# Optimization experiments

Measured on AMD Instinct MI355X. Metric: run time of the kernel, lower is better.

Reference implementation:

```python
import jax, jax.numpy as jnp
import numpy as np

B, T, F, H = 64, 2048, 128, 32  # batch, seq_len, input_features, lstm hidden


def setup_inputs() -> dict:
    key = jax.random.key(0)
    ks = jax.random.split(key, 4)
    X = jax.random.normal(ks[0], (B, T, F), dtype=jnp.float32)
    # combined gate weights, order (i, f, g, o) as in flax.linen.LSTMCell
    Wx = jax.random.normal(ks[1], (F, 4 * H), dtype=jnp.float32) / np.float32(np.sqrt(F))
    Wh = jax.random.normal(ks[2], (H, 4 * H), dtype=jnp.float32) / np.float32(np.sqrt(H))
    b = jnp.zeros((4 * H,), dtype=jnp.float32)
    Wd = jax.random.normal(ks[3], (H, 1), dtype=jnp.float32) / np.float32(np.sqrt(H))
    bd = jnp.zeros((1,), dtype=jnp.float32)
    return {"X": X, "Wx": Wx, "Wh": Wh, "b": b, "Wd": Wd, "bd": bd}


def reference(X, Wx, Wh, b, Wd, bd):
    # Precompute input->gate projections for all timesteps in one GEMM.
    xg = jnp.einsum('btf,fg->btg', X, Wx) + b  # [B, T, 4H]

    def step(carry, xg_t):
        c, h = carry
        g = xg_t + h @ Wh  # [B, 4H]
        i, f, gc, o = jnp.split(g, 4, axis=-1)
        c = jax.nn.sigmoid(f) * c + jax.nn.sigmoid(i) * jnp.tanh(gc)
        h = jax.nn.sigmoid(o) * jnp.tanh(c)
        return (c, h), None

    zeros = jnp.zeros((X.shape[0], H), X.dtype)
    (c_T, h_T), _ = jax.lax.scan(step, (zeros, zeros), jnp.swapaxes(xg, 0, 1))
    # Dense(1) applied to outputs, then last timestep selected == Dense on h_T
    return h_T @ Wd + bd  # [B, 1]
```

## Files before the change

### kernel.cpp

```cpp
#include <hip/hip_runtime.h>
#include <math.h>

#define BB 64
#define TT 2048
#define FF 128
#define HH 32
#define GG 128

#define S1f (-1.4426950408889634f)
#define S2f (-2.8853900817779268f)

__global__ __launch_bounds__(256) void xg_gemm(const float* __restrict__ X,
                                               const float* __restrict__ Wx,
                                               const float* __restrict__ bias,
                                               float* __restrict__ xgT) {
    __shared__ float XL[64 * 32];
    __shared__ float WL[32 * 128];
    const int tid = threadIdx.x;
    const int row0 = blockIdx.x * 64;
    const int j0 = (tid & 15) * 8;
    const int r0 = (tid >> 4) * 4;

    float acc[4][8];
#pragma unroll
    for (int r = 0; r < 4; ++r)
#pragma unroll
        for (int jj = 0; jj < 8; ++jj) acc[r][jj] = 0.f;

    for (int f0 = 0; f0 < FF; f0 += 32) {
        __syncthreads();
        {
            const float4* src = (const float4*)(Wx + f0 * GG);
            float4* dst = (float4*)WL;
            dst[tid]       = src[tid];
            dst[tid + 256] = src[tid + 256];
            dst[tid + 512] = src[tid + 512];
            dst[tid + 768] = src[tid + 768];
        }
        {
            int lin = tid * 4;
            int row = lin >> 5;
            int fi  = lin & 31;
            ((float4*)XL)[tid] =
                *(const float4*)(X + (size_t)(row0 + row) * FF + f0 + fi);
            lin = (tid + 256) * 4;
            row = lin >> 5;
            fi  = lin & 31;
            ((float4*)XL)[tid + 256] =
                *(const float4*)(X + (size_t)(row0 + row) * FF + f0 + fi);
        }
        __syncthreads();
#pragma unroll 4
        for (int fi = 0; fi < 32; ++fi) {
            float xv[4];
#pragma unroll
            for (int r = 0; r < 4; ++r) xv[r] = XL[(r0 + r) * 32 + fi];
            float4 w0 = *(float4*)&WL[fi * GG + j0];
            float4 w1 = *(float4*)&WL[fi * GG + j0 + 4];
            float w[8] = {w0.x, w0.y, w0.z, w0.w, w1.x, w1.y, w1.z, w1.w};
#pragma unroll
            for (int r = 0; r < 4; ++r)
#pragma unroll
                for (int jj = 0; jj < 8; ++jj)
                    acc[r][jj] = fmaf(xv[r], w[jj], acc[r][jj]);
        }
    }
    const int b  = row0 >> 11;
    const int t0 = (row0 & 2047) + r0;
    float bl[8];
#pragma unroll
    for (int jj = 0; jj < 8; ++jj) bl[jj] = bias[j0 + jj];
#pragma unroll
    for (int jj = 0; jj < 8; ++jj) {
        const int j = j0 + jj;
        const float sc = (j >= 64 && j < 96) ? S2f : S1f;
        float4 o;
        o.x = (acc[0][jj] + bl[jj]) * sc;
        o.y = (acc[1][jj] + bl[jj]) * sc;
        o.z = (acc[2][jj] + bl[jj]) * sc;
        o.w = (acc[3][jj] + bl[jj]) * sc;
        *(float4*)(xgT + ((size_t)b * GG + j) * TT + t0) = o;
    }
}

__device__ __forceinline__ float rcp_(float x) { return __builtin_amdgcn_rcpf(x); }
__device__ __forceinline__ float exp2_(float x) { return __builtin_amdgcn_exp2f(x); }

__global__ __launch_bounds__(64) void lstm_rec(const float* __restrict__ xgT,
                                               const float* __restrict__ Wh,
                                               const float* __restrict__ Wd,
                                               const float* __restrict__ bd,
                                               float* __restrict__ out) {
    const int b = blockIdx.x;
    const int l = threadIdx.x;
    const bool lo = (l < HH);

    const float scx = S1f;
    const float scy = lo ? S2f : S1f;
    float2 wh[HH];
#pragma unroll
    for (int k = 0; k < HH; ++k)
        wh[k] = make_float2(Wh[k * GG + l] * scx, Wh[k * GG + l + 64] * scy);

    const float A1 = lo ? 2.f : 1.f;
    const float B1 = lo ? -1.f : 0.f;

    float h = 0.f;
    float c = 0.f;

    const float* pX = xgT + ((size_t)b * GG + l) * TT;
    const float* pY = xgT + ((size_t)b * GG + l + 64) * TT;

    float4 curX = *(const float4*)(pX);
    float4 curY = *(const float4*)(pY);
    float4 nxtX = *(const float4*)(pX + 4);
    float4 nxtY = *(const float4*)(pY + 4);

    auto step = [&](float xi, float xy) __attribute__((always_inline)) {
        float ax[4] = {xi, 0.f, 0.f, 0.f};
        float ay[4] = {xy, 0.f, 0.f, 0.f};
#pragma unroll
        for (int kc = 0; kc < 4; ++kc) {
#pragma unroll
            for (int k = 0; k < 8; ++k) {
                const int kk = kc * 8 + k;
                float hk = __uint_as_float(
                    __builtin_amdgcn_readlane(__float_as_uint(h), kk));
                ax[kc] = fmaf(hk, wh[kk].x, ax[kc]);
                ay[kc] = fmaf(hk, wh[kk].y, ay[kc]);
            }
        }
        float a0 = (ax[0] + ax[1]) + (ax[2] + ax[3]);
        float a1 = (ay[0] + ay[1]) + (ay[2] + ay[3]);

        float act0 = rcp_(1.f + exp2_(a0));
        float act1 = fmaf(A1, rcp_(1.f + exp2_(a1)), B1);

        auto pq = __builtin_amdgcn_permlane32_swap(__float_as_uint(act0),
                                                   __float_as_uint(act1), false, false);
        auto uv = __builtin_amdgcn_permlane32_swap(__float_as_uint(act1),
                                                   __float_as_uint(act0), false, false);
        float p = __uint_as_float(pq[0]);
        float q = __uint_as_float(pq[1]);
        float u = __uint_as_float(uv[0]);
        float v = __uint_as_float(uv[1]);

        float f_all = lo ? q : act0;
        float o_all = lo ? v : act1;
        c = fmaf(f_all, c, u * p);
        float tc = fmaf(2.f, rcp_(1.f + exp2_(c * S2f)), -1.f);
        h = o_all * tc;
    };

#pragma unroll 1
    for (int t4 = 0; t4 < TT; t4 += 4) {
        float4 uX = curX, uY = curY;
        curX = nxtX; curY = nxtY;
        if (t4 + 8 < TT) {
            nxtX = *(const float4*)(pX + t4 + 8);
            nxtY = *(const float4*)(pY + t4 + 8);
        }
        step(uX.x, uY.x);
        step(uX.y, uY.y);
        step(uX.z, uY.z);
        step(uX.w, uY.w);
    }

    float contrib = h * Wd[l & (HH - 1)];
#pragma unroll
    for (int off = 32; off >= 1; off >>= 1)
        contrib += __shfl_xor(contrib, off, 64);
    if (l == 0) out[b] = fmaf(0.5f, contrib, bd[0]);
}

extern "C" void kernel_launch(void* const* d_in, const int* in_sizes, int n_in,
                              void* d_out, int out_size, void* d_ws, size_t ws_size,
                              hipStream_t stream) {
    const float* X    = (const float*)d_in[0];
    const float* Wx   = (const float*)d_in[1];
    const float* Wh   = (const float*)d_in[2];
    const float* bias = (const float*)d_in[3];
    const float* Wd   = (const float*)d_in[4];
    const float* bd   = (const float*)d_in[5];
    float* out = (float*)d_out;
    float* xgT = (float*)d_ws;

    hipLaunchKernelGGL(xg_gemm, dim3((BB * TT) / 64), dim3(256), 0, stream,
                       X, Wx, bias, xgT);
    hipLaunchKernelGGL(lstm_rec, dim3(BB), dim3(64), 0, stream,
                       xgT, Wh, Wd, bd, out);
}
```

Measured before the change: 523.1 us.

## Use packed fp16 dot2 for recurrent matvec and interleave two batches per wave

Recurrent weights are packed into fp16 pairs, and h is paired with its neighbouring lane via DPP, so the 32-term matvec becomes 16 fdot2 ops with half the readlanes. Each wave now runs two independent batch sequences whose steps are interleaved to hide dependency latency, and the launch uses half as many blocks. This lowers per-step instruction count and latency on the serial critical path. The cost is fp16 rounding of weights and hidden state, which lowers accuracy.

```diff
diff --git a/kernel.cpp b/kernel.cpp
--- a/kernel.cpp
+++ b/kernel.cpp
@@ -9,6 +9,21 @@
 
 #define S1f (-1.4426950408889634f)
 #define S2f (-2.8853900817779268f)
+
+typedef _Float16 half2_t __attribute__((ext_vector_type(2)));
+
+__device__ __forceinline__ unsigned h2u(half2_t v) {
+    unsigned u; __builtin_memcpy(&u, &v, 4); return u;
+}
+__device__ __forceinline__ half2_t u2h(unsigned u) {
+    half2_t v; __builtin_memcpy(&v, &u, 4); return v;
+}
+__device__ __forceinline__ half2_t pkrtz(float a, float b) {
+    auto r = __builtin_amdgcn_cvt_pkrtz(a, b);
+    half2_t v; __builtin_memcpy(&v, &r, 4); return v;
+}
+__device__ __forceinline__ float rcp_(float x) { return __builtin_amdgcn_rcpf(x); }
+__device__ __forceinline__ float exp2_(float x) { return __builtin_amdgcn_exp2f(x); }
 
 __global__ __launch_bounds__(256) void xg_gemm(const float* __restrict__ X,
                                                const float* __restrict__ Wx,
@@ -83,52 +98,64 @@
     }
 }
 
-__device__ __forceinline__ float rcp_(float x) { return __builtin_amdgcn_rcpf(x); }
-__device__ __forceinline__ float exp2_(float x) { return __builtin_amdgcn_exp2f(x); }
-
 __global__ __launch_bounds__(64) void lstm_rec(const float* __restrict__ xgT,
                                                const float* __restrict__ Wh,
                                                const float* __restrict__ Wd,
                                                const float* __restrict__ bd,
                                                float* __restrict__ out) {
-    const int b = blockIdx.x;
     const int l = threadIdx.x;
     const bool lo = (l < HH);
+    const int b0 = blockIdx.x * 2;
+    const int b1 = b0 + 1;
 
     const float scx = S1f;
     const float scy = lo ? S2f : S1f;
-    float2 wh[HH];
-#pragma unroll
-    for (int k = 0; k < HH; ++k)
-        wh[k] = make_float2(Wh[k * GG + l] * scx, Wh[k * GG + l + 64] * scy);
+    half2_t whx[16], why[16];
+#pragma unroll
+    for (int k = 0; k < 16; ++k) {
+        float w0 = Wh[(2 * k) * GG + l] * scx;
+        float w1 = Wh[(2 * k + 1) * GG + l] * scx;
+        whx[k] = pkrtz(w0, w1);
+        float v0 = Wh[(2 * k) * GG + l + 64] * scy;
+        float v1 = Wh[(2 * k + 1) * GG + l + 64] * scy;
+        why[k] = pkrtz(v0, v1);
+    }
 
     const float A1 = lo ? 2.f : 1.f;
     const float B1 = lo ? -1.f : 0.f;
 
-    float h = 0.f;
-    float c = 0.f;
-
-    const float* pX = xgT + ((size_t)b * GG + l) * TT;
-    const float* pY = xgT + ((size_t)b * GG + l + 64) * TT;
-
-    float4 curX = *(const float4*)(pX);
-    float4 curY = *(const float4*)(pY);
-    float4 nxtX = *(const float4*)(pX + 4);
-    float4 nxtY = *(const float4*)(pY + 4);
-
-    auto step = [&](float xi, float xy) __attribute__((always_inline)) {
+    float hA = 0.f, cA = 0.f;
+    float hB = 0.f, cB = 0.f;
+
+    const float* pXA = xgT + ((size_t)b0 * GG + l) * TT;
+    const float* pYA = xgT + ((size_t)b0 * GG + l + 64) * TT;
+    const float* pXB = xgT + ((size_t)b1 * GG + l) * TT;
+    const float* pYB = xgT + ((size_t)b1 * GG + l + 64) * TT;
+
+    float4 curXA = *(const float4*)(pXA);
+    float4 curYA = *(const float4*)(pYA);
+    float4 curXB = *(const float4*)(pXB);
+    float4 curYB = *(const float4*)(pYB);
+    float4 nxtXA = *(const float4*)(pXA + 4);
+    float4 nxtYA = *(const float4*)(pYA + 4);
+    float4 nxtXB = *(const float4*)(pXB + 4);
+    float4 nxtYB = *(const float4*)(pYB + 4);
+
+    auto step = [&](float& h, float& c, float xi, float xy)
+        __attribute__((always_inline)) {
+        unsigned hu = __float_as_uint(h);
+        unsigned hxu = (unsigned)__builtin_amdgcn_mov_dpp(
+            (int)hu, 0xB1 , 0xF, 0xF, true);
+        half2_t hp = pkrtz(h, __uint_as_float(hxu));
+        unsigned hpu = h2u(hp);
+
         float ax[4] = {xi, 0.f, 0.f, 0.f};
         float ay[4] = {xy, 0.f, 0.f, 0.f};
 #pragma unroll
-        for (int kc = 0; kc < 4; ++kc) {
-#pragma unroll
-            for (int k = 0; k < 8; ++k) {
-                const int kk = kc * 8 + k;
-                float hk = __uint_as_float(
-                    __builtin_amdgcn_readlane(__float_as_uint(h), kk));
-                ax[kc] = fmaf(hk, wh[kk].x, ax[kc]);
-                ay[kc] = fmaf(hk, wh[kk].y, ay[kc]);
-            }
+        for (int k = 0; k < 16; ++k) {
+            half2_t s = u2h(__builtin_amdgcn_readlane(hpu, 2 * k));
+            ax[k & 3] = __builtin_amdgcn_fdot2(s, whx[k], ax[k & 3], false);
+            ay[k & 3] = __builtin_amdgcn_fdot2(s, why[k], ay[k & 3], false);
         }
         float a0 = (ax[0] + ax[1]) + (ax[2] + ax[3]);
         float a1 = (ay[0] + ay[1]) + (ay[2] + ay[3]);
@@ -154,23 +181,32 @@
 
 #pragma unroll 1
     for (int t4 = 0; t4 < TT; t4 += 4) {
-        float4 uX = curX, uY = curY;
-        curX = nxtX; curY = nxtY;
+        float4 uXA = curXA, uYA = curYA, uXB = curXB, uYB = curYB;
+        curXA = nxtXA; curYA = nxtYA; curXB = nxtXB; curYB = nxtYB;
         if (t4 + 8 < TT) {
-            nxtX = *(const float4*)(pX + t4 + 8);
-            nxtY = *(const float4*)(pY + t4 + 8);
-        }
-        step(uX.x, uY.x);
-        step(uX.y, uY.y);
-        step(uX.z, uY.z);
-        step(uX.w, uY.w);
-    }
-
-    float contrib = h * Wd[l & (HH - 1)];
-#pragma unroll
-    for (int off = 32; off >= 1; off >>= 1)
-        contrib += __shfl_xor(contrib, off, 64);
-    if (l == 0) out[b] = fmaf(0.5f, contrib, bd[0]);
+            nxtXA = *(const float4*)(pXA + t4 + 8);
+            nxtYA = *(const float4*)(pYA + t4 + 8);
+            nxtXB = *(const float4*)(pXB + t4 + 8);
+            nxtYB = *(const float4*)(pYB + t4 + 8);
+        }
+        step(hA, cA, uXA.x, uYA.x);  step(hB, cB, uXB.x, uYB.x);
+        step(hA, cA, uXA.y, uYA.y);  step(hB, cB, uXB.y, uYB.y);
+        step(hA, cA, uXA.z, uYA.z);  step(hB, cB, uXB.z, uYB.z);
+        step(hA, cA, uXA.w, uYA.w);  step(hB, cB, uXB.w, uYB.w);
+    }
+
+    const float wd = Wd[l & (HH - 1)];
+    float ca = hA * wd;
+    float cb = hB * wd;
+#pragma unroll
+    for (int off = 32; off >= 1; off >>= 1) {
+        ca += __shfl_xor(ca, off, 64);
+        cb += __shfl_xor(cb, off, 64);
+    }
+    if (l == 0) {
+        out[b0] = fmaf(0.5f, ca, bd[0]);
+        out[b1] = fmaf(0.5f, cb, bd[0]);
+    }
 }
 
 extern "C" void kernel_launch(void* const* d_in, const int* in_sizes, int n_in,
@@ -187,6 +223,6 @@
 
     hipLaunchKernelGGL(xg_gemm, dim3((BB * TT) / 64), dim3(256), 0, stream,
                        X, Wx, bias, xgT);
-    hipLaunchKernelGGL(lstm_rec, dim3(BB), dim3(64), 0, stream,
+    hipLaunchKernelGGL(lstm_rec, dim3(BB / 2), dim3(64), 0, stream,
                        xgT, Wh, Wd, bd, out);
 }
```

Result: slower. 1.000 ms (+91.2%).

## Use packed fp16 dot2 with DPP/swizzle h broadcast in LSTM recurrence

Applied to the files above, without the earlier changes.

Replaces the 32 per-step readlane broadcasts of h with one fp16 pair pack followed by a tree of DPP and ds_swizzle permutations. Each lane then receives 16 distinct h-pairs. Wh is pre-permuted to match and packed into half2, so the matvec uses 16 fdot2 ops per gate half instead of 32 fp32 FMAs. The goal is a shorter serial critical path per timestep, at the cost of fp16 rounding of h and Wh (round-toward-zero), which may hurt accuracy over 2048 steps.

```diff
diff --git a/kernel.cpp b/kernel.cpp
--- a/kernel.cpp
+++ b/kernel.cpp
@@ -9,6 +9,29 @@
 
 #define S1f (-1.4426950408889634f)
 #define S2f (-2.8853900817779268f)
+
+typedef _Float16 half2_t __attribute__((ext_vector_type(2)));
+
+__device__ __forceinline__ unsigned h2u(half2_t v) {
+    unsigned u; __builtin_memcpy(&u, &v, 4); return u;
+}
+__device__ __forceinline__ half2_t u2h(unsigned u) {
+    half2_t v; __builtin_memcpy(&v, &u, 4); return v;
+}
+__device__ __forceinline__ half2_t pkrtz(float a, float b) {
+    auto r = __builtin_amdgcn_cvt_pkrtz(a, b);
+    half2_t v; __builtin_memcpy(&v, &r, 4); return v;
+}
+__device__ __forceinline__ float rcp_(float x) { return __builtin_amdgcn_rcpf(x); }
+__device__ __forceinline__ float exp2_(float x) { return __builtin_amdgcn_exp2f(x); }
+
+#define DPP_(x, ctrl) \
+    ((unsigned)__builtin_amdgcn_mov_dpp((int)(x), (ctrl), 0xF, 0xF, true))
+#define CTRL_XOR1 0xB1
+#define CTRL_XOR2 0x4E
+#define CTRL_ROR4 0x124
+#define CTRL_ROR8 0x128
+#define SWZ16_(x) ((unsigned)__builtin_amdgcn_ds_swizzle((int)(x), 0x401F))
 
 __global__ __launch_bounds__(256) void xg_gemm(const float* __restrict__ X,
                                                const float* __restrict__ Wx,
@@ -83,24 +106,36 @@
     }
 }
 
-__device__ __forceinline__ float rcp_(float x) { return __builtin_amdgcn_rcpf(x); }
-__device__ __forceinline__ float exp2_(float x) { return __builtin_amdgcn_exp2f(x); }
-
 __global__ __launch_bounds__(64) void lstm_rec(const float* __restrict__ xgT,
                                                const float* __restrict__ Wh,
                                                const float* __restrict__ Wd,
                                                const float* __restrict__ bd,
                                                float* __restrict__ out) {
+    const int l = threadIdx.x;
+    const int m = l & 31;
+    const bool lo = (l < HH);
     const int b = blockIdx.x;
-    const int l = threadIdx.x;
-    const bool lo = (l < HH);
+
+    unsigned iv[16];
+    iv[0] = (unsigned)m;
+    iv[1] = SWZ16_(iv[0]);
+    iv[2] = DPP_(iv[0], CTRL_XOR2);
+    iv[3] = DPP_(iv[1], CTRL_XOR2);
+#pragma unroll
+    for (int r = 0; r < 4; ++r) iv[4 + r] = DPP_(iv[r], CTRL_ROR4);
+#pragma unroll
+    for (int r = 0; r < 8; ++r) iv[8 + r] = DPP_(iv[r], CTRL_ROR8);
 
     const float scx = S1f;
     const float scy = lo ? S2f : S1f;
-    float2 wh[HH];
-#pragma unroll
-    for (int k = 0; k < HH; ++k)
-        wh[k] = make_float2(Wh[k * GG + l] * scx, Wh[k * GG + l + 64] * scy);
+    half2_t whx[16], why[16];
+#pragma unroll
+    for (int r = 0; r < 16; ++r) {
+        const int p  = (int)(iv[r] & 31u);
+        const int p2 = p ^ 1;
+        whx[r] = pkrtz(Wh[p * GG + l] * scx,       Wh[p2 * GG + l] * scx);
+        why[r] = pkrtz(Wh[p * GG + l + 64] * scy,  Wh[p2 * GG + l + 64] * scy);
+    }
 
     const float A1 = lo ? 2.f : 1.f;
     const float B1 = lo ? -1.f : 0.f;
@@ -117,18 +152,24 @@
     float4 nxtY = *(const float4*)(pY + 4);
 
     auto step = [&](float xi, float xy) __attribute__((always_inline)) {
+        unsigned g[16];
+        unsigned hn = DPP_(__float_as_uint(h), CTRL_XOR1);
+        g[0] = h2u(pkrtz(h, __uint_as_float(hn)));
+        g[1] = SWZ16_(g[0]);
+        g[2] = DPP_(g[0], CTRL_XOR2);
+        g[3] = DPP_(g[1], CTRL_XOR2);
+#pragma unroll
+        for (int r = 0; r < 4; ++r) g[4 + r] = DPP_(g[r], CTRL_ROR4);
+#pragma unroll
+        for (int r = 0; r < 8; ++r) g[8 + r] = DPP_(g[r], CTRL_ROR8);
+
         float ax[4] = {xi, 0.f, 0.f, 0.f};
         float ay[4] = {xy, 0.f, 0.f, 0.f};
 #pragma unroll
-        for (int kc = 0; kc < 4; ++kc) {
-#pragma unroll
-            for (int k = 0; k < 8; ++k) {
-                const int kk = kc * 8 + k;
-                float hk = __uint_as_float(
-                    __builtin_amdgcn_readlane(__float_as_uint(h), kk));
-                ax[kc] = fmaf(hk, wh[kk].x, ax[kc]);
-                ay[kc] = fmaf(hk, wh[kk].y, ay[kc]);
-            }
+        for (int r = 0; r < 16; ++r) {
+            half2_t hp = u2h(g[r]);
+            ax[r & 3] = __builtin_amdgcn_fdot2(hp, whx[r], ax[r & 3], false);
+            ay[r & 3] = __builtin_amdgcn_fdot2(hp, why[r], ay[r & 3], false);
         }
         float a0 = (ax[0] + ax[1]) + (ax[2] + ax[3]);
         float a1 = (ay[0] + ay[1]) + (ay[2] + ay[3]);
@@ -166,7 +207,7 @@
         step(uX.w, uY.w);
     }
 
-    float contrib = h * Wd[l & (HH - 1)];
+    float contrib = h * Wd[m];
 #pragma unroll
     for (int off = 32; off >= 1; off >>= 1)
         contrib += __shfl_xor(contrib, off, 64);
```

Result: faster. 509.5 us (-2.6%).
